# Kernel optimization log

Measured on AMD Instinct MI355X. Metric: run time of the kernel, lower is better.

The kernel has to match this reference:

```python
import jax, jax.numpy as jnp
import numpy as np

EPS = 0.5          # entropy_epsilon
TAU = 0.5          # tau = 1 * entropy_epsilon
MAXITER = 10

NABLA_W = np.array([[[[0., 0., 0.], [0., -1., 0.], [0., 1., 0.]]],
                    [[[0., 0., 0.], [0., -1., 1.], [0., 0., 0.]]]], dtype=np.float32)  # (2,1,3,3)
DIV_W = np.array([[[[0., -1., 0.], [0., 1., 0.], [0., 0., 0.]],
                   [[0., 0., 0.], [-1., 1., 0.], [0., 0., 0.]]]], dtype=np.float32)    # (1,2,3,3)


def _conv(x, w):
    # x: (B,C,H,W), w: (O,I,3,3), padding=1 -> SAME
    return jax.lax.conv_general_dilated(
        x, w, window_strides=(1, 1), padding='SAME',
        dimension_numbers=('NCHW', 'OIHW', 'NCHW'))


def setup_inputs() -> dict:
    key = jax.random.key(0)
    k1, k2 = jax.random.split(key)
    B, H, W = 8, 1024, 1024
    o = jax.random.normal(k1, (B, 1, H, W), dtype=jnp.float32)
    vector_field = jax.random.normal(k2, (H, W, 2), dtype=jnp.float32)
    nabla_w = jnp.asarray(NABLA_W)
    div_w = jnp.asarray(DIV_W)
    return {"o": o, "vector_field": vector_field, "nabla_w": nabla_w, "div_w": div_w}


def reference(o, vector_field, nabla_w, div_w):
    o = o[:, 0]                      # (B,H,W)
    vf1 = vector_field[:, :, 1]      # (H,W)
    vf0 = vector_field[:, :, 0]      # (H,W)
    u = jax.nn.sigmoid(o / EPS)
    q = jnp.zeros_like(o)
    Tq = jnp.zeros_like(o)
    for _ in range(MAXITER):
        u_nabla = _conv(u[:, None], nabla_w)          # (B,2,H,W)
        q = q - TAU * (u_nabla[:, 0] * vf1 + u_nabla[:, 1] * vf0)
        q = jnp.maximum(q, 0.0)
        Tq = _conv(jnp.stack([vf1 * q, vf0 * q], axis=1), div_w)[:, 0]  # (B,H,W)
        u = jax.nn.sigmoid((o - Tq) / EPS)
    u1 = (o - Tq) / EPS
    return u1
```

## Files before the change

### kernel.cpp

```cpp
#include <hip/hip_runtime.h>
#include <math.h>

#define IMG_H 1024
#define IMG_W 1024
#define IMG_B 8
#define TPB 256
#define RPB 16
#define BANDS (IMG_H / RPB)
#define NBLK (IMG_B * BANDS)

__device__ __forceinline__ float sig2(float x) {
    return 1.0f / (1.0f + __expf(-2.0f * x));
}

__global__ __launch_bounds__(TPB) void k_fused2(const float* __restrict__ qin,
                                                const float* __restrict__ vf,
                                                const float* __restrict__ o,
                                                float* __restrict__ qout) {
    __shared__ __align__(16) float spa[IMG_W + 4];
    __shared__ __align__(16) float su0[2][IMG_W + 4];
    __shared__ __align__(16) float spb[IMG_W + 4];
    __shared__ __align__(16) float su1[2][IMG_W + 4];

    const int img  = blockIdx.x / BANDS;
    const int r0   = (blockIdx.x % BANDS) * RPB;
    const int x0   = threadIdx.x * 4;
    const bool topb = (r0 == 0);
    const size_t ibase = (size_t)img * IMG_H * IMG_W;

    const int ylo  = topb ? 0 : r0 - 2;
    const int yhi  = (r0 + RPB + 1 < IMG_H) ? r0 + RPB + 1 : IMG_H - 1;
    const int yend = r0 + RPB + 1;
    const int u_lo = topb ? 0 : r0 - 1;

    float qc[4], oc4[4], v0c[4], v1c[4];
    float qn[4], on4[4], v0n[4], v1n[4];
    float p1prev[4] = {0,0,0,0};
    float qz[4], oz4[4], v0z[4], v1z[4];
    float v0w[4], v1w[4];
    float qpz[4], qpw[4];
    float p0pz[4], p1pz[4];
    float p1pprev[4] = {0,0,0,0};

    {
        const size_t rb = ibase + (size_t)ylo * IMG_W + x0;
        float4 q4 = *(const float4*)(qin + rb);
        float4 o4 = *(const float4*)(o + rb);
        const size_t vb = ((size_t)ylo * IMG_W + x0) * 2;
        float4 va = *(const float4*)(vf + vb);
        float4 vb4 = *(const float4*)(vf + vb + 4);
        qc[0]=q4.x; qc[1]=q4.y; qc[2]=q4.z; qc[3]=q4.w;
        oc4[0]=o4.x; oc4[1]=o4.y; oc4[2]=o4.z; oc4[3]=o4.w;
        v0c[0]=va.x; v0c[1]=va.z; v0c[2]=vb4.x; v0c[3]=vb4.z;
        v1c[0]=va.y; v1c[1]=va.w; v1c[2]=vb4.y; v1c[3]=vb4.w;
    }

    for (int y = ylo; y <= yend; ++y) {
        if (y + 1 <= yhi) {
            const size_t rb = ibase + (size_t)(y + 1) * IMG_W + x0;
            float4 q4 = *(const float4*)(qin + rb);
            float4 o4 = *(const float4*)(o + rb);
            const size_t vb = ((size_t)(y + 1) * IMG_W + x0) * 2;
            float4 va = *(const float4*)(vf + vb);
            float4 vb4 = *(const float4*)(vf + vb + 4);
            qn[0]=q4.x; qn[1]=q4.y; qn[2]=q4.z; qn[3]=q4.w;
            on4[0]=o4.x; on4[1]=o4.y; on4[2]=o4.z; on4[3]=o4.w;
            v0n[0]=va.x; v0n[1]=va.z; v0n[2]=vb4.x; v0n[3]=vb4.z;
            v1n[0]=va.y; v1n[1]=va.w; v1n[2]=vb4.y; v1n[3]=vb4.w;
        } else {
#pragma unroll
            for (int j = 0; j < 4; ++j) { qn[j]=0.f; on4[j]=0.f; v0n[j]=0.f; v1n[j]=0.f; }
        }

        float p0c[4], p1c[4];
        const bool have_y = (y <= yhi);
        if (have_y) {
#pragma unroll
            for (int j = 0; j < 4; ++j) {
                p0c[j] = v0c[j] * qc[j];
                p1c[j] = v1c[j] * qc[j];
                spa[x0 + 1 + j] = p0c[j];
            }
            if (threadIdx.x == 0) spa[0] = 0.0f;
        } else {
#pragma unroll
            for (int j = 0; j < 4; ++j) { p0c[j] = 0.f; p1c[j] = 0.f; }
        }
        __syncthreads();

        const int buf0 = y & 1;
        if (y >= u_lo) {
            if (y <= IMG_H - 1) {
#pragma unroll
                for (int j = 0; j < 4; ++j) {
                    float Tq = p1c[j] - p1prev[j] + p0c[j] - spa[x0 + j];
                    su0[buf0][x0 + j] = sig2(oc4[j] - Tq);
                }
            } else {
#pragma unroll
                for (int j = 0; j < 4; ++j) su0[buf0][x0 + j] = 0.0f;
            }
            if (threadIdx.x == 0) su0[buf0][IMG_W] = 0.0f;
        }
        __syncthreads();

        const int z = y - 1;
        const bool s3 = (z >= u_lo) && (z <= r0 + RPB) && (z <= IMG_H - 1);
        if (s3) {
            const int zb = z & 1;
#pragma unroll
            for (int j = 0; j < 4; ++j) {
                float gy = su0[buf0][x0 + j] - su0[zb][x0 + j];
                float gx = su0[zb][x0 + j + 1] - su0[zb][x0 + j];
                qpz[j] = fmaxf(qz[j] - 0.5f * (gy * v1z[j] + gx * v0z[j]), 0.0f);
            }
#pragma unroll
            for (int j = 0; j < 4; ++j) {
                p0pz[j] = v0z[j] * qpz[j];
                p1pz[j] = v1z[j] * qpz[j];
                spb[x0 + 1 + j] = p0pz[j];
            }
            if (threadIdx.x == 0) spb[0] = 0.0f;
        }
        __syncthreads();

        if (z >= r0 && z <= r0 + RPB) {
            const int zb = z & 1;
            if (z <= IMG_H - 1) {
#pragma unroll
                for (int j = 0; j < 4; ++j) {
                    float Tq = p1pz[j] - p1pprev[j] + p0pz[j] - spb[x0 + j];
                    su1[zb][x0 + j] = sig2(oz4[j] - Tq);
                }
            } else {
#pragma unroll
                for (int j = 0; j < 4; ++j) su1[zb][x0 + j] = 0.0f;
            }
            if (threadIdx.x == 0) su1[zb][IMG_W] = 0.0f;
        }
        __syncthreads();

        const int w = y - 2;
        if (w >= r0 && w <= r0 + RPB - 1) {
            const int wb = w & 1, wb1 = 1 - wb;
            float r[4];
#pragma unroll
            for (int j = 0; j < 4; ++j) {
                float gy = su1[wb1][x0 + j] - su1[wb][x0 + j];
                float gx = su1[wb][x0 + j + 1] - su1[wb][x0 + j];
                r[j] = fmaxf(qpw[j] - 0.5f * (gy * v1w[j] + gx * v0w[j]), 0.0f);
            }
            *(float4*)(qout + ibase + (size_t)w * IMG_W + x0) =
                make_float4(r[0], r[1], r[2], r[3]);
        }

#pragma unroll
        for (int j = 0; j < 4; ++j) {
            p1prev[j] = p1c[j];
            v0w[j] = v0z[j]; v1w[j] = v1z[j];
            qz[j] = qc[j]; oz4[j] = oc4[j]; v0z[j] = v0c[j]; v1z[j] = v1c[j];
            qc[j] = qn[j]; oc4[j] = on4[j]; v0c[j] = v0n[j]; v1c[j] = v1n[j];
        }
        if (s3) {
#pragma unroll
            for (int j = 0; j < 4; ++j) { qpw[j] = qpz[j]; p1pprev[j] = p1pz[j]; }
        }
    }
}

__global__ __launch_bounds__(TPB) void k_init2(const float* __restrict__ o,
                                               const float* __restrict__ vf,
                                               float* __restrict__ qout) {
    __shared__ __align__(16) float su0[2][IMG_W + 4];
    __shared__ __align__(16) float spb[IMG_W + 4];
    __shared__ __align__(16) float su1[2][IMG_W + 4];

    const int img  = blockIdx.x / BANDS;
    const int r0   = (blockIdx.x % BANDS) * RPB;
    const int x0   = threadIdx.x * 4;
    const bool topb = (r0 == 0);
    const size_t ibase = (size_t)img * IMG_H * IMG_W;

    const int u_lo = topb ? 0 : r0 - 1;
    const int ylo  = u_lo;
    const int yhi  = (r0 + RPB + 1 < IMG_H) ? r0 + RPB + 1 : IMG_H - 1;
    const int yend = r0 + RPB + 1;

    float oc4[4], v0c[4], v1c[4];
    float on4[4], v0n[4], v1n[4];
    float oz4[4], v0z[4], v1z[4];
    float v0w[4], v1w[4];
    float qpz[4], qpw[4];
    float p0pz[4], p1pz[4];
    float p1pprev[4] = {0,0,0,0};

    {
        const size_t rb = ibase + (size_t)ylo * IMG_W + x0;
        float4 o4 = *(const float4*)(o + rb);
        const size_t vb = ((size_t)ylo * IMG_W + x0) * 2;
        float4 va = *(const float4*)(vf + vb);
        float4 vb4 = *(const float4*)(vf + vb + 4);
        oc4[0]=o4.x; oc4[1]=o4.y; oc4[2]=o4.z; oc4[3]=o4.w;
        v0c[0]=va.x; v0c[1]=va.z; v0c[2]=vb4.x; v0c[3]=vb4.z;
        v1c[0]=va.y; v1c[1]=va.w; v1c[2]=vb4.y; v1c[3]=vb4.w;
    }

    for (int y = ylo; y <= yend; ++y) {
        if (y + 1 <= yhi) {
            const size_t rb = ibase + (size_t)(y + 1) * IMG_W + x0;
            float4 o4 = *(const float4*)(o + rb);
            const size_t vb = ((size_t)(y + 1) * IMG_W + x0) * 2;
            float4 va = *(const float4*)(vf + vb);
            float4 vb4 = *(const float4*)(vf + vb + 4);
            on4[0]=o4.x; on4[1]=o4.y; on4[2]=o4.z; on4[3]=o4.w;
            v0n[0]=va.x; v0n[1]=va.z; v0n[2]=vb4.x; v0n[3]=vb4.z;
            v1n[0]=va.y; v1n[1]=va.w; v1n[2]=vb4.y; v1n[3]=vb4.w;
        } else {
#pragma unroll
            for (int j = 0; j < 4; ++j) { on4[j]=0.f; v0n[j]=0.f; v1n[j]=0.f; }
        }

        const int buf0 = y & 1;
        if (y <= IMG_H - 1) {
#pragma unroll
            for (int j = 0; j < 4; ++j) su0[buf0][x0 + j] = sig2(oc4[j]);
        } else {
#pragma unroll
            for (int j = 0; j < 4; ++j) su0[buf0][x0 + j] = 0.0f;
        }
        if (threadIdx.x == 0) su0[buf0][IMG_W] = 0.0f;
        __syncthreads();

        const int z = y - 1;
        const bool s3 = (z >= u_lo) && (z <= r0 + RPB) && (z <= IMG_H - 1);
        if (s3) {
            const int zb = z & 1;
#pragma unroll
            for (int j = 0; j < 4; ++j) {
                float gy = su0[buf0][x0 + j] - su0[zb][x0 + j];
                float gx = su0[zb][x0 + j + 1] - su0[zb][x0 + j];
                qpz[j] = fmaxf(-0.5f * (gy * v1z[j] + gx * v0z[j]), 0.0f);
            }
#pragma unroll
            for (int j = 0; j < 4; ++j) {
                p0pz[j] = v0z[j] * qpz[j];
                p1pz[j] = v1z[j] * qpz[j];
                spb[x0 + 1 + j] = p0pz[j];
            }
            if (threadIdx.x == 0) spb[0] = 0.0f;
        }
        __syncthreads();

        if (z >= r0 && z <= r0 + RPB) {
            const int zb = z & 1;
            if (z <= IMG_H - 1) {
#pragma unroll
                for (int j = 0; j < 4; ++j) {
                    float Tq = p1pz[j] - p1pprev[j] + p0pz[j] - spb[x0 + j];
                    su1[zb][x0 + j] = sig2(oz4[j] - Tq);
                }
            } else {
#pragma unroll
                for (int j = 0; j < 4; ++j) su1[zb][x0 + j] = 0.0f;
            }
            if (threadIdx.x == 0) su1[zb][IMG_W] = 0.0f;
        }
        __syncthreads();

        const int w = y - 2;
        if (w >= r0 && w <= r0 + RPB - 1) {
            const int wb = w & 1, wb1 = 1 - wb;
            float r[4];
#pragma unroll
            for (int j = 0; j < 4; ++j) {
                float gy = su1[wb1][x0 + j] - su1[wb][x0 + j];
                float gx = su1[wb][x0 + j + 1] - su1[wb][x0 + j];
                r[j] = fmaxf(qpw[j] - 0.5f * (gy * v1w[j] + gx * v0w[j]), 0.0f);
            }
            *(float4*)(qout + ibase + (size_t)w * IMG_W + x0) =
                make_float4(r[0], r[1], r[2], r[3]);
        }

#pragma unroll
        for (int j = 0; j < 4; ++j) {
            v0w[j] = v0z[j]; v1w[j] = v1z[j];
            oz4[j] = oc4[j]; v0z[j] = v0c[j]; v1z[j] = v1c[j];
            oc4[j] = on4[j]; v0c[j] = v0n[j]; v1c[j] = v1n[j];
        }
        if (s3) {
#pragma unroll
            for (int j = 0; j < 4; ++j) { qpw[j] = qpz[j]; p1pprev[j] = p1pz[j]; }
        }
    }
}

__global__ __launch_bounds__(TPB) void k_final(const float* __restrict__ q,
                                               const float* __restrict__ vf,
                                               const float* __restrict__ o,
                                               float* __restrict__ out) {
    __shared__ __align__(16) float sp0[IMG_W + 4];
    const int row = blockIdx.x & (IMG_H - 1);
    const int x0  = threadIdx.x * 4;
    const size_t base = (size_t)blockIdx.x * IMG_W;

    float4 q4 = *(const float4*)(q + base + x0);
    const size_t vbase = ((size_t)row * IMG_W + x0) * 2;
    float4 vfa = *(const float4*)(vf + vbase);
    float4 vfb = *(const float4*)(vf + vbase + 4);

    const float v0[4] = {vfa.x, vfa.z, vfb.x, vfb.z};
    const float v1[4] = {vfa.y, vfa.w, vfb.y, vfb.w};
    const float qc[4] = {q4.x, q4.y, q4.z, q4.w};

    float p0[4], p1[4];
#pragma unroll
    for (int j = 0; j < 4; ++j) {
        p0[j] = v0[j] * qc[j];
        p1[j] = v1[j] * qc[j];
        sp0[x0 + j + 1] = p0[j];
    }
    if (threadIdx.x == 0) sp0[0] = 0.0f;

    float p1m[4];
    if (row > 0) {
        float4 qm  = *(const float4*)(q + base - IMG_W + x0);
        float4 vma = *(const float4*)(vf + vbase - 2 * IMG_W);
        float4 vmb = *(const float4*)(vf + vbase - 2 * IMG_W + 4);
        p1m[0] = qm.x * vma.y; p1m[1] = qm.y * vma.w;
        p1m[2] = qm.z * vmb.y; p1m[3] = qm.w * vmb.w;
    } else {
        p1m[0] = p1m[1] = p1m[2] = p1m[3] = 0.0f;
    }

    float4 o4 = *(const float4*)(o + base + x0);
    const float oc[4] = {o4.x, o4.y, o4.z, o4.w};

    __syncthreads();

    float r[4];
#pragma unroll
    for (int j = 0; j < 4; ++j) {
        float Tq = p1[j] - p1m[j] + p0[j] - sp0[x0 + j];
        r[j] = 2.0f * (oc[j] - Tq);
    }
    *(float4*)(out + base + x0) = make_float4(r[0], r[1], r[2], r[3]);
}

extern "C" void kernel_launch(void* const* d_in, const int* in_sizes, int n_in,
                              void* d_out, int out_size, void* d_ws, size_t ws_size,
                              hipStream_t stream) {
    const float* o  = (const float*)d_in[0];
    const float* vf = (const float*)d_in[1];

    float* qA = (float*)d_ws;
    float* qB = (float*)d_out;

    k_init2 <<<NBLK, TPB, 0, stream>>>(o, vf, qA);
    k_fused2<<<NBLK, TPB, 0, stream>>>(qA, vf, o, qB);
    k_fused2<<<NBLK, TPB, 0, stream>>>(qB, vf, o, qA);
    k_fused2<<<NBLK, TPB, 0, stream>>>(qA, vf, o, qB);
    k_fused2<<<NBLK, TPB, 0, stream>>>(qB, vf, o, qA);
    k_final <<<IMG_B * IMG_H, TPB, 0, stream>>>(qA, vf, o, (float*)d_out);
}
```

Measured before the change: 269.6 us.

## Fuse five solver iterations per kernel with a templated deep row pipeline

Replaces the init, four two-iteration fused kernels and the final kernel with a templated pipelined kernel. Each launch runs five iterations in a rolling row wavefront, so only two launches are needed. The final Tq/output step is folded into the second launch. Neighbour exchange now goes through a per-thread 4-wide shared buffer holding only boundary values. This cuts global q round trips and launch count, at the cost of larger recomputed halos (five rows per side), more registers, and more barriers per row.

```diff
diff --git a/kernel.cpp b/kernel.cpp
--- a/kernel.cpp
+++ b/kernel.cpp
@@ -12,338 +12,230 @@
 __device__ __forceinline__ float sig2(float x) {
     return 1.0f / (1.0f + __expf(-2.0f * x));
 }
-
-__global__ __launch_bounds__(TPB) void k_fused2(const float* __restrict__ qin,
-                                                const float* __restrict__ vf,
-                                                const float* __restrict__ o,
-                                                float* __restrict__ qout) {
-    __shared__ __align__(16) float spa[IMG_W + 4];
-    __shared__ __align__(16) float su0[2][IMG_W + 4];
-    __shared__ __align__(16) float spb[IMG_W + 4];
-    __shared__ __align__(16) float su1[2][IMG_W + 4];
-
-    const int img  = blockIdx.x / BANDS;
-    const int r0   = (blockIdx.x % BANDS) * RPB;
-    const int x0   = threadIdx.x * 4;
-    const bool topb = (r0 == 0);
+__device__ __forceinline__ int imax(int a, int b) { return a > b ? a : b; }
+__device__ __forceinline__ int imin(int a, int b) { return a < b ? a : b; }
+
+template<int D, bool READQ, bool FINAL>
+__global__ __launch_bounds__(TPB, 2) void k_pipe(const float* __restrict__ qin,
+                                                 const float* __restrict__ vf,
+                                                 const float* __restrict__ o,
+                                                 float* __restrict__ out) {
+    __shared__ float sp[D + 1][TPB + 1];
+    __shared__ float su[D][2][TPB + 1];
+
+    const int img = blockIdx.x / BANDS;
+    const int r0  = (blockIdx.x % BANDS) * RPB;
+    const int tid = threadIdx.x;
+    const int x0  = tid * 4;
     const size_t ibase = (size_t)img * IMG_H * IMG_W;
 
-    const int ylo  = topb ? 0 : r0 - 2;
-    const int yhi  = (r0 + RPB + 1 < IMG_H) ? r0 + RPB + 1 : IMG_H - 1;
-    const int yend = r0 + RPB + 1;
-    const int u_lo = topb ? 0 : r0 - 1;
-
-    float qc[4], oc4[4], v0c[4], v1c[4];
-    float qn[4], on4[4], v0n[4], v1n[4];
-    float p1prev[4] = {0,0,0,0};
-    float qz[4], oz4[4], v0z[4], v1z[4];
-    float v0w[4], v1w[4];
-    float qpz[4], qpw[4];
-    float p0pz[4], p1pz[4];
-    float p1pprev[4] = {0,0,0,0};
+    if (tid == 0) {
+#pragma unroll
+        for (int l = 0; l <= D; ++l) sp[l][0] = 0.0f;
+#pragma unroll
+        for (int l = 0; l < D; ++l) { su[l][0][TPB] = 0.0f; su[l][1][TPB] = 0.0f; }
+    }
+
+    constexpr int HALO = FINAL ? 1 : 0;
+    constexpr int NOH  = FINAL ? D + 1 : D;
+
+    const int u0lo = imax(r0 - (D - 1) - HALO, 0);
+    const int ylo  = READQ ? imax(r0 - D - HALO, 0) : u0lo;
+    const int yend = r0 + RPB - 1 + D;
+    const int yhi  = imin(yend, IMG_H - 1);
+
+    float qc[4], qn[4], qz[4];
+    float oh[NOH][4], on[4];
+    float v0h[D + 1][4], v1h[D + 1][4], v0n[4], v1n[4];
+    float uY[D][4], uZ[D][4];
+    float p1prev[D + 1][4];
+    float qsave[D][4];
+    float qvPrev[4];
+
+#pragma unroll
+    for (int j = 0; j < 4; ++j) {
+        qc[j]=qn[j]=qz[j]=on[j]=v0n[j]=v1n[j]=qvPrev[j]=0.0f;
+#pragma unroll
+        for (int l = 0; l < NOH; ++l) oh[l][j] = 0.0f;
+#pragma unroll
+        for (int l = 0; l <= D; ++l) { v0h[l][j]=0.0f; v1h[l][j]=0.0f; p1prev[l][j]=0.0f; }
+#pragma unroll
+        for (int l = 0; l < D; ++l) { uY[l][j]=0.0f; uZ[l][j]=0.0f; qsave[l][j]=0.0f; }
+    }
 
     {
         const size_t rb = ibase + (size_t)ylo * IMG_W + x0;
-        float4 q4 = *(const float4*)(qin + rb);
+        if constexpr (READQ) {
+            float4 q4 = *(const float4*)(qin + rb);
+            qc[0]=q4.x; qc[1]=q4.y; qc[2]=q4.z; qc[3]=q4.w;
+        }
         float4 o4 = *(const float4*)(o + rb);
+        oh[0][0]=o4.x; oh[0][1]=o4.y; oh[0][2]=o4.z; oh[0][3]=o4.w;
         const size_t vb = ((size_t)ylo * IMG_W + x0) * 2;
         float4 va = *(const float4*)(vf + vb);
         float4 vb4 = *(const float4*)(vf + vb + 4);
-        qc[0]=q4.x; qc[1]=q4.y; qc[2]=q4.z; qc[3]=q4.w;
-        oc4[0]=o4.x; oc4[1]=o4.y; oc4[2]=o4.z; oc4[3]=o4.w;
-        v0c[0]=va.x; v0c[1]=va.z; v0c[2]=vb4.x; v0c[3]=vb4.z;
-        v1c[0]=va.y; v1c[1]=va.w; v1c[2]=vb4.y; v1c[3]=vb4.w;
+        v0h[0][0]=va.x; v0h[0][1]=va.z; v0h[0][2]=vb4.x; v0h[0][3]=vb4.z;
+        v1h[0][0]=va.y; v1h[0][1]=va.w; v1h[0][2]=vb4.y; v1h[0][3]=vb4.w;
     }
 
     for (int y = ylo; y <= yend; ++y) {
         if (y + 1 <= yhi) {
             const size_t rb = ibase + (size_t)(y + 1) * IMG_W + x0;
-            float4 q4 = *(const float4*)(qin + rb);
+            if constexpr (READQ) {
+                float4 q4 = *(const float4*)(qin + rb);
+                qn[0]=q4.x; qn[1]=q4.y; qn[2]=q4.z; qn[3]=q4.w;
+            }
             float4 o4 = *(const float4*)(o + rb);
+            on[0]=o4.x; on[1]=o4.y; on[2]=o4.z; on[3]=o4.w;
             const size_t vb = ((size_t)(y + 1) * IMG_W + x0) * 2;
             float4 va = *(const float4*)(vf + vb);
             float4 vb4 = *(const float4*)(vf + vb + 4);
-            qn[0]=q4.x; qn[1]=q4.y; qn[2]=q4.z; qn[3]=q4.w;
-            on4[0]=o4.x; on4[1]=o4.y; on4[2]=o4.z; on4[3]=o4.w;
             v0n[0]=va.x; v0n[1]=va.z; v0n[2]=vb4.x; v0n[3]=vb4.z;
             v1n[0]=va.y; v1n[1]=va.w; v1n[2]=vb4.y; v1n[3]=vb4.w;
         } else {
 #pragma unroll
-            for (int j = 0; j < 4; ++j) { qn[j]=0.f; on4[j]=0.f; v0n[j]=0.f; v1n[j]=0.f; }
-        }
-
-        float p0c[4], p1c[4];
-        const bool have_y = (y <= yhi);
-        if (have_y) {
+            for (int j = 0; j < 4; ++j) { qn[j]=0.f; on[j]=0.f; v0n[j]=0.f; v1n[j]=0.f; }
+        }
+
+        if constexpr (READQ) {
+            float p0c[4], p1c[4];
+            const bool haveY = (y <= yhi);
+            if (haveY) {
+#pragma unroll
+                for (int j = 0; j < 4; ++j) { p0c[j]=v0h[0][j]*qc[j]; p1c[j]=v1h[0][j]*qc[j]; }
+                sp[0][tid + 1] = p0c[3];
+            } else {
+#pragma unroll
+                for (int j = 0; j < 4; ++j) { p0c[j]=0.f; p1c[j]=0.f; }
+            }
+            __syncthreads();
+            if (y >= u0lo) {
+                const float lft = sp[0][tid];
+#pragma unroll
+                for (int j = 0; j < 4; ++j) {
+                    float pm1 = (j == 0) ? lft : p0c[j - 1];
+                    float nu = (y <= IMG_H - 1)
+                        ? sig2(oh[0][j] - (p1c[j] - p1prev[0][j] + p0c[j] - pm1)) : 0.0f;
+                    uZ[0][j] = uY[0][j]; uY[0][j] = nu;
+                }
+                su[0][y & 1][tid] = uY[0][0];
+            }
+#pragma unroll
+            for (int j = 0; j < 4; ++j) p1prev[0][j] = p1c[j];
+        } else {
 #pragma unroll
             for (int j = 0; j < 4; ++j) {
-                p0c[j] = v0c[j] * qc[j];
-                p1c[j] = v1c[j] * qc[j];
-                spa[x0 + 1 + j] = p0c[j];
-            }
-            if (threadIdx.x == 0) spa[0] = 0.0f;
-        } else {
-#pragma unroll
-            for (int j = 0; j < 4; ++j) { p0c[j] = 0.f; p1c[j] = 0.f; }
-        }
-        __syncthreads();
-
-        const int buf0 = y & 1;
-        if (y >= u_lo) {
-            if (y <= IMG_H - 1) {
+                float nu = (y <= IMG_H - 1) ? sig2(oh[0][j]) : 0.0f;
+                uZ[0][j] = uY[0][j]; uY[0][j] = nu;
+            }
+            su[0][y & 1][tid] = uY[0][0];
+        }
+
+#pragma unroll
+        for (int l = 1; l <= D; ++l) {
+            const int t = y - l;
+            const int qlo = imax(r0 - (D - l) - HALO, 0);
+            const bool qvalid = (t >= qlo) && (t <= IMG_H - 1);
+            float qbase[4], qv[4];
+#pragma unroll
+            for (int j = 0; j < 4; ++j)
+                qbase[j] = (l == 1) ? (READQ ? qz[j] : 0.0f) : qsave[l - 1][j];
+            if (l >= 2) {
+#pragma unroll
+                for (int j = 0; j < 4; ++j) qsave[l - 1][j] = qvPrev[j];
+            }
+            if (qvalid) {
+                const float uR = su[l - 1][t & 1][tid + 1];
 #pragma unroll
                 for (int j = 0; j < 4; ++j) {
-                    float Tq = p1c[j] - p1prev[j] + p0c[j] - spa[x0 + j];
-                    su0[buf0][x0 + j] = sig2(oc4[j] - Tq);
+                    float gy = uY[l - 1][j] - uZ[l - 1][j];
+                    float gx = ((j < 3) ? uZ[l - 1][j + 1] : uR) - uZ[l - 1][j];
+                    qv[j] = fmaxf(qbase[j] - 0.5f * (gy * v1h[l][j] + gx * v0h[l][j]), 0.0f);
                 }
             } else {
 #pragma unroll
-                for (int j = 0; j < 4; ++j) su0[buf0][x0 + j] = 0.0f;
-            }
-            if (threadIdx.x == 0) su0[buf0][IMG_W] = 0.0f;
-        }
-        __syncthreads();
-
-        const int z = y - 1;
-        const bool s3 = (z >= u_lo) && (z <= r0 + RPB) && (z <= IMG_H - 1);
-        if (s3) {
-            const int zb = z & 1;
-#pragma unroll
-            for (int j = 0; j < 4; ++j) {
-                float gy = su0[buf0][x0 + j] - su0[zb][x0 + j];
-                float gx = su0[zb][x0 + j + 1] - su0[zb][x0 + j];
-                qpz[j] = fmaxf(qz[j] - 0.5f * (gy * v1z[j] + gx * v0z[j]), 0.0f);
-            }
-#pragma unroll
-            for (int j = 0; j < 4; ++j) {
-                p0pz[j] = v0z[j] * qpz[j];
-                p1pz[j] = v1z[j] * qpz[j];
-                spb[x0 + 1 + j] = p0pz[j];
-            }
-            if (threadIdx.x == 0) spb[0] = 0.0f;
-        }
-        __syncthreads();
-
-        if (z >= r0 && z <= r0 + RPB) {
-            const int zb = z & 1;
-            if (z <= IMG_H - 1) {
-#pragma unroll
-                for (int j = 0; j < 4; ++j) {
-                    float Tq = p1pz[j] - p1pprev[j] + p0pz[j] - spb[x0 + j];
-                    su1[zb][x0 + j] = sig2(oz4[j] - Tq);
-                }
+                for (int j = 0; j < 4; ++j) qv[j] = 0.0f;
+            }
+
+            if (l < D) {
+                float p0p[4], p1p[4];
+                if (qvalid) {
+#pragma unroll
+                    for (int j = 0; j < 4; ++j) { p0p[j]=v0h[l][j]*qv[j]; p1p[j]=v1h[l][j]*qv[j]; }
+                    sp[l][tid + 1] = p0p[3];
+                } else {
+#pragma unroll
+                    for (int j = 0; j < 4; ++j) { p0p[j]=0.f; p1p[j]=0.f; }
+                }
+                __syncthreads();
+                const int ulo = imax(r0 - (D - 1 - l) - HALO, 0);
+                if (t >= ulo) {
+                    const float lft = sp[l][tid];
+#pragma unroll
+                    for (int j = 0; j < 4; ++j) {
+                        float pm1 = (j == 0) ? lft : p0p[j - 1];
+                        float nu = (t <= IMG_H - 1)
+                            ? sig2(oh[l][j] - (p1p[j] - p1prev[l][j] + p0p[j] - pm1)) : 0.0f;
+                        uZ[l][j] = uY[l][j]; uY[l][j] = nu;
+                    }
+                    su[l][t & 1][tid] = uY[l][0];
+                }
+#pragma unroll
+                for (int j = 0; j < 4; ++j) p1prev[l][j] = p1p[j];
             } else {
-#pragma unroll
-                for (int j = 0; j < 4; ++j) su1[zb][x0 + j] = 0.0f;
-            }
-            if (threadIdx.x == 0) su1[zb][IMG_W] = 0.0f;
-        }
-        __syncthreads();
-
-        const int w = y - 2;
-        if (w >= r0 && w <= r0 + RPB - 1) {
-            const int wb = w & 1, wb1 = 1 - wb;
-            float r[4];
-#pragma unroll
-            for (int j = 0; j < 4; ++j) {
-                float gy = su1[wb1][x0 + j] - su1[wb][x0 + j];
-                float gx = su1[wb][x0 + j + 1] - su1[wb][x0 + j];
-                r[j] = fmaxf(qpw[j] - 0.5f * (gy * v1w[j] + gx * v0w[j]), 0.0f);
-            }
-            *(float4*)(qout + ibase + (size_t)w * IMG_W + x0) =
-                make_float4(r[0], r[1], r[2], r[3]);
-        }
-
-#pragma unroll
-        for (int j = 0; j < 4; ++j) {
-            p1prev[j] = p1c[j];
-            v0w[j] = v0z[j]; v1w[j] = v1z[j];
-            qz[j] = qc[j]; oz4[j] = oc4[j]; v0z[j] = v0c[j]; v1z[j] = v1c[j];
-            qc[j] = qn[j]; oc4[j] = on4[j]; v0c[j] = v0n[j]; v1c[j] = v1n[j];
-        }
-        if (s3) {
-#pragma unroll
-            for (int j = 0; j < 4; ++j) { qpw[j] = qpz[j]; p1pprev[j] = p1pz[j]; }
-        }
-    }
-}
-
-__global__ __launch_bounds__(TPB) void k_init2(const float* __restrict__ o,
-                                               const float* __restrict__ vf,
-                                               float* __restrict__ qout) {
-    __shared__ __align__(16) float su0[2][IMG_W + 4];
-    __shared__ __align__(16) float spb[IMG_W + 4];
-    __shared__ __align__(16) float su1[2][IMG_W + 4];
-
-    const int img  = blockIdx.x / BANDS;
-    const int r0   = (blockIdx.x % BANDS) * RPB;
-    const int x0   = threadIdx.x * 4;
-    const bool topb = (r0 == 0);
-    const size_t ibase = (size_t)img * IMG_H * IMG_W;
-
-    const int u_lo = topb ? 0 : r0 - 1;
-    const int ylo  = u_lo;
-    const int yhi  = (r0 + RPB + 1 < IMG_H) ? r0 + RPB + 1 : IMG_H - 1;
-    const int yend = r0 + RPB + 1;
-
-    float oc4[4], v0c[4], v1c[4];
-    float on4[4], v0n[4], v1n[4];
-    float oz4[4], v0z[4], v1z[4];
-    float v0w[4], v1w[4];
-    float qpz[4], qpw[4];
-    float p0pz[4], p1pz[4];
-    float p1pprev[4] = {0,0,0,0};
-
-    {
-        const size_t rb = ibase + (size_t)ylo * IMG_W + x0;
-        float4 o4 = *(const float4*)(o + rb);
-        const size_t vb = ((size_t)ylo * IMG_W + x0) * 2;
-        float4 va = *(const float4*)(vf + vb);
-        float4 vb4 = *(const float4*)(vf + vb + 4);
-        oc4[0]=o4.x; oc4[1]=o4.y; oc4[2]=o4.z; oc4[3]=o4.w;
-        v0c[0]=va.x; v0c[1]=va.z; v0c[2]=vb4.x; v0c[3]=vb4.z;
-        v1c[0]=va.y; v1c[1]=va.w; v1c[2]=vb4.y; v1c[3]=vb4.w;
-    }
-
-    for (int y = ylo; y <= yend; ++y) {
-        if (y + 1 <= yhi) {
-            const size_t rb = ibase + (size_t)(y + 1) * IMG_W + x0;
-            float4 o4 = *(const float4*)(o + rb);
-            const size_t vb = ((size_t)(y + 1) * IMG_W + x0) * 2;
-            float4 va = *(const float4*)(vf + vb);
-            float4 vb4 = *(const float4*)(vf + vb + 4);
-            on4[0]=o4.x; on4[1]=o4.y; on4[2]=o4.z; on4[3]=o4.w;
-            v0n[0]=va.x; v0n[1]=va.z; v0n[2]=vb4.x; v0n[3]=vb4.z;
-            v1n[0]=va.y; v1n[1]=va.w; v1n[2]=vb4.y; v1n[3]=vb4.w;
-        } else {
-#pragma unroll
-            for (int j = 0; j < 4; ++j) { on4[j]=0.f; v0n[j]=0.f; v1n[j]=0.f; }
-        }
-
-        const int buf0 = y & 1;
-        if (y <= IMG_H - 1) {
-#pragma unroll
-            for (int j = 0; j < 4; ++j) su0[buf0][x0 + j] = sig2(oc4[j]);
-        } else {
-#pragma unroll
-            for (int j = 0; j < 4; ++j) su0[buf0][x0 + j] = 0.0f;
-        }
-        if (threadIdx.x == 0) su0[buf0][IMG_W] = 0.0f;
-        __syncthreads();
-
-        const int z = y - 1;
-        const bool s3 = (z >= u_lo) && (z <= r0 + RPB) && (z <= IMG_H - 1);
-        if (s3) {
-            const int zb = z & 1;
-#pragma unroll
-            for (int j = 0; j < 4; ++j) {
-                float gy = su0[buf0][x0 + j] - su0[zb][x0 + j];
-                float gx = su0[zb][x0 + j + 1] - su0[zb][x0 + j];
-                qpz[j] = fmaxf(-0.5f * (gy * v1z[j] + gx * v0z[j]), 0.0f);
-            }
-#pragma unroll
-            for (int j = 0; j < 4; ++j) {
-                p0pz[j] = v0z[j] * qpz[j];
-                p1pz[j] = v1z[j] * qpz[j];
-                spb[x0 + 1 + j] = p0pz[j];
-            }
-            if (threadIdx.x == 0) spb[0] = 0.0f;
-        }
-        __syncthreads();
-
-        if (z >= r0 && z <= r0 + RPB) {
-            const int zb = z & 1;
-            if (z <= IMG_H - 1) {
-#pragma unroll
-                for (int j = 0; j < 4; ++j) {
-                    float Tq = p1pz[j] - p1pprev[j] + p0pz[j] - spb[x0 + j];
-                    su1[zb][x0 + j] = sig2(oz4[j] - Tq);
-                }
-            } else {
-#pragma unroll
-                for (int j = 0; j < 4; ++j) su1[zb][x0 + j] = 0.0f;
-            }
-            if (threadIdx.x == 0) su1[zb][IMG_W] = 0.0f;
-        }
-        __syncthreads();
-
-        const int w = y - 2;
-        if (w >= r0 && w <= r0 + RPB - 1) {
-            const int wb = w & 1, wb1 = 1 - wb;
-            float r[4];
-#pragma unroll
-            for (int j = 0; j < 4; ++j) {
-                float gy = su1[wb1][x0 + j] - su1[wb][x0 + j];
-                float gx = su1[wb][x0 + j + 1] - su1[wb][x0 + j];
-                r[j] = fmaxf(qpw[j] - 0.5f * (gy * v1w[j] + gx * v0w[j]), 0.0f);
-            }
-            *(float4*)(qout + ibase + (size_t)w * IMG_W + x0) =
-                make_float4(r[0], r[1], r[2], r[3]);
-        }
-
-#pragma unroll
-        for (int j = 0; j < 4; ++j) {
-            v0w[j] = v0z[j]; v1w[j] = v1z[j];
-            oz4[j] = oc4[j]; v0z[j] = v0c[j]; v1z[j] = v1c[j];
-            oc4[j] = on4[j]; v0c[j] = v0n[j]; v1c[j] = v1n[j];
-        }
-        if (s3) {
-#pragma unroll
-            for (int j = 0; j < 4; ++j) { qpw[j] = qpz[j]; p1pprev[j] = p1pz[j]; }
-        }
-    }
-}
-
-__global__ __launch_bounds__(TPB) void k_final(const float* __restrict__ q,
-                                               const float* __restrict__ vf,
-                                               const float* __restrict__ o,
-                                               float* __restrict__ out) {
-    __shared__ __align__(16) float sp0[IMG_W + 4];
-    const int row = blockIdx.x & (IMG_H - 1);
-    const int x0  = threadIdx.x * 4;
-    const size_t base = (size_t)blockIdx.x * IMG_W;
-
-    float4 q4 = *(const float4*)(q + base + x0);
-    const size_t vbase = ((size_t)row * IMG_W + x0) * 2;
-    float4 vfa = *(const float4*)(vf + vbase);
-    float4 vfb = *(const float4*)(vf + vbase + 4);
-
-    const float v0[4] = {vfa.x, vfa.z, vfb.x, vfb.z};
-    const float v1[4] = {vfa.y, vfa.w, vfb.y, vfb.w};
-    const float qc[4] = {q4.x, q4.y, q4.z, q4.w};
-
-    float p0[4], p1[4];
-#pragma unroll
-    for (int j = 0; j < 4; ++j) {
-        p0[j] = v0[j] * qc[j];
-        p1[j] = v1[j] * qc[j];
-        sp0[x0 + j + 1] = p0[j];
-    }
-    if (threadIdx.x == 0) sp0[0] = 0.0f;
-
-    float p1m[4];
-    if (row > 0) {
-        float4 qm  = *(const float4*)(q + base - IMG_W + x0);
-        float4 vma = *(const float4*)(vf + vbase - 2 * IMG_W);
-        float4 vmb = *(const float4*)(vf + vbase - 2 * IMG_W + 4);
-        p1m[0] = qm.x * vma.y; p1m[1] = qm.y * vma.w;
-        p1m[2] = qm.z * vmb.y; p1m[3] = qm.w * vmb.w;
-    } else {
-        p1m[0] = p1m[1] = p1m[2] = p1m[3] = 0.0f;
-    }
-
-    float4 o4 = *(const float4*)(o + base + x0);
-    const float oc[4] = {o4.x, o4.y, o4.z, o4.w};
-
-    __syncthreads();
-
-    float r[4];
-#pragma unroll
-    for (int j = 0; j < 4; ++j) {
-        float Tq = p1[j] - p1m[j] + p0[j] - sp0[x0 + j];
-        r[j] = 2.0f * (oc[j] - Tq);
-    }
-    *(float4*)(out + base + x0) = make_float4(r[0], r[1], r[2], r[3]);
+                if constexpr (FINAL) {
+                    float p0p[4], p1p[4];
+                    if (qvalid) {
+#pragma unroll
+                        for (int j = 0; j < 4; ++j) { p0p[j]=v0h[D][j]*qv[j]; p1p[j]=v1h[D][j]*qv[j]; }
+                        sp[D][tid + 1] = p0p[3];
+                    } else {
+#pragma unroll
+                        for (int j = 0; j < 4; ++j) { p0p[j]=0.f; p1p[j]=0.f; }
+                    }
+                    __syncthreads();
+                    if (t >= r0 && t < r0 + RPB) {
+                        const float lft = sp[D][tid];
+                        float r[4];
+#pragma unroll
+                        for (int j = 0; j < 4; ++j) {
+                            float pm1 = (j == 0) ? lft : p0p[j - 1];
+                            float Tq = p1p[j] - p1prev[D][j] + p0p[j] - pm1;
+                            r[j] = 2.0f * (oh[D][j] - Tq);
+                        }
+                        *(float4*)(out + ibase + (size_t)t * IMG_W + x0) =
+                            make_float4(r[0], r[1], r[2], r[3]);
+                    }
+#pragma unroll
+                    for (int j = 0; j < 4; ++j) p1prev[D][j] = p1p[j];
+                } else {
+                    if (t >= r0 && t < r0 + RPB) {
+                        *(float4*)(out + ibase + (size_t)t * IMG_W + x0) =
+                            make_float4(qv[0], qv[1], qv[2], qv[3]);
+                    }
+                }
+            }
+#pragma unroll
+            for (int j = 0; j < 4; ++j) qvPrev[j] = qv[j];
+        }
+
+#pragma unroll
+        for (int k = D; k >= 1; --k)
+#pragma unroll
+            for (int j = 0; j < 4; ++j) { v0h[k][j]=v0h[k-1][j]; v1h[k][j]=v1h[k-1][j]; }
+#pragma unroll
+        for (int j = 0; j < 4; ++j) { v0h[0][j]=v0n[j]; v1h[0][j]=v1n[j]; }
+#pragma unroll
+        for (int k = NOH - 1; k >= 1; --k)
+#pragma unroll
+            for (int j = 0; j < 4; ++j) oh[k][j] = oh[k-1][j];
+#pragma unroll
+        for (int j = 0; j < 4; ++j) oh[0][j] = on[j];
+        if constexpr (READQ) {
+#pragma unroll
+            for (int j = 0; j < 4; ++j) { qz[j] = qc[j]; qc[j] = qn[j]; }
+        }
+    }
 }
 
 extern "C" void kernel_launch(void* const* d_in, const int* in_sizes, int n_in,
@@ -351,14 +243,8 @@
                               hipStream_t stream) {
     const float* o  = (const float*)d_in[0];
     const float* vf = (const float*)d_in[1];
-
     float* qA = (float*)d_ws;
-    float* qB = (float*)d_out;
-
-    k_init2 <<<NBLK, TPB, 0, stream>>>(o, vf, qA);
-    k_fused2<<<NBLK, TPB, 0, stream>>>(qA, vf, o, qB);
-    k_fused2<<<NBLK, TPB, 0, stream>>>(qB, vf, o, qA);
-    k_fused2<<<NBLK, TPB, 0, stream>>>(qA, vf, o, qB);
-    k_fused2<<<NBLK, TPB, 0, stream>>>(qB, vf, o, qA);
-    k_final <<<IMG_B * IMG_H, TPB, 0, stream>>>(qA, vf, o, (float*)d_out);
+
+    k_pipe<5, false, false><<<NBLK, TPB, 0, stream>>>(o, vf, o, qA);
+    k_pipe<5, true,  true ><<<NBLK, TPB, 0, stream>>>(qA, vf, o, (float*)d_out);
 }
```

After: 251.2 us. -6.8%, faster.
